# Kernel tuning notes

Measured on AMD Instinct MI355X. Metric: run time of the kernel, lower is better.

Reference implementation:

```python
import jax, jax.numpy as jnp
import numpy as np

N_EX = 50000          # n_exercise
D = 128               # exercise_embed_dim
E = 600000            # number of e2e edges
N = N_EX + 1          # node count: zero pad row + exercises 1..n_exercise


def setup_inputs() -> dict:
    key = jax.random.key(0)
    k1, k2, k3, k4, k5 = jax.random.split(key, 5)
    # learned params
    W_embed = jax.random.normal(k1, (N, D), dtype=jnp.float32) * 0.02   # nn.Embedding(n_exercise+1, D)
    W_gcn = jax.random.normal(k2, (D, D), dtype=jnp.float32) * (1.0 / np.sqrt(D))  # GCNConv lin weight
    b_gcn = jnp.zeros((D,), dtype=jnp.float32)                          # GCNConv bias
    # graph / sequence inputs
    edge_index = jax.random.randint(k3, (2, E), 0, N, dtype=jnp.int64)
    e_inputs = jax.random.randint(k4, (16, 200), 0, N_EX, dtype=jnp.int64)
    a_inputs = jax.random.randint(k5, (16, 200), 0, 2, dtype=jnp.int64)
    return {"W_embed": W_embed, "W_gcn": W_gcn, "b_gcn": b_gcn,
            "edge_index": edge_index, "e_inputs": e_inputs, "a_inputs": a_inputs}


def reference(W_embed, W_gcn, b_gcn, edge_index, e_inputs, a_inputs):
    n_nodes, d = W_embed.shape
    # exercise_embed = embed(arange(1, n_exercise+1)); prepend zero row ->
    # equivalent to the full table with row 0 zeroed.
    x = W_embed.at[0].set(0.0)                        # [N, D]

    # PyG GCNConv: h = x @ W, then D^-1/2 (A + I) D^-1/2 h + b
    h = x @ W_gcn                                     # [N, D]
    src = edge_index[0]
    dst = edge_index[1]
    ones_e = jnp.ones(src.shape[0], dtype=h.dtype)
    # degree including self-loop weight 1
    deg = 1.0 + jax.ops.segment_sum(ones_e, dst, num_segments=n_nodes)  # [N]
    dis = jax.lax.rsqrt(deg)                          # deg^-1/2
    norm = dis[src] * dis[dst]                        # [E]
    msg = h[src] * norm[:, None]                      # gather + scale, [E, D]
    agg = jax.ops.segment_sum(msg, dst, num_segments=n_nodes)           # scatter-add, [N, D]
    agg = agg + h * (1.0 / deg)[:, None]              # self-loop term (norm = 1/deg)
    return agg + b_gcn                                # [N, D]
```

## Files before the change

kernel.cpp:

```cpp
#include <hip/hip_runtime.h>

#define N_NODES 50001
#define DIM 128
#define GEMM_BLOCKS 782
#define CAP 64
#define NB 196
#define FILLB 293
#define EPB 2048
#define BCAP 40
#define GCAPR 640
#define OCAP 8192

typedef __attribute__((ext_vector_type(8))) short short8v;
typedef __attribute__((ext_vector_type(4))) float f32x4;

__device__ __forceinline__ ushort f2bf(float f) {
    unsigned u = __float_as_uint(f);
    unsigned r = (u + 0x7FFF + ((u >> 16) & 1)) >> 16;
    return (ushort)r;
}

__global__ void prep_kernel(int* __restrict__ gcntp, int* __restrict__ ocnt,
                            const float* __restrict__ Wg, ushort* __restrict__ wt) {
    __shared__ float tile[32][36];
    const int t = threadIdx.x;
    if (blockIdx.x == 0) {
        for (int i = t; i < NB * 8 * 16; i += 256) gcntp[i] = 0;
        if (t == 0) *ocnt = 0;
        return;
    }
    const int b2 = blockIdx.x - 1;
    const int bk = b2 >> 2;
    const int bn = b2 & 3;
    {
        int k = bk * 32 + (t >> 3);
        int n = bn * 32 + (t & 7) * 4;
        float4 v = *(const float4*)&Wg[(size_t)k * DIM + n];
        tile[t >> 3][(t & 7) * 4 + 0] = v.x;
        tile[t >> 3][(t & 7) * 4 + 1] = v.y;
        tile[t >> 3][(t & 7) * 4 + 2] = v.z;
        tile[t >> 3][(t & 7) * 4 + 3] = v.w;
    }
    __syncthreads();
    {
        int n = bn * 32 + (t >> 3);
        int k = bk * 32 + (t & 7) * 4;
        ushort4 w4;
        w4.x = f2bf(tile[(t & 7) * 4 + 0][t >> 3]);
        w4.y = f2bf(tile[(t & 7) * 4 + 1][t >> 3]);
        w4.z = f2bf(tile[(t & 7) * 4 + 2][t >> 3]);
        w4.w = f2bf(tile[(t & 7) * 4 + 3][t >> 3]);
        *(ushort4*)&wt[(size_t)n * DIM + k] = w4;
    }
}

__launch_bounds__(256)
__global__ void gemm_fill_kernel(const float* __restrict__ X, const ushort* __restrict__ wt,
                                 ushort* __restrict__ h16,
                                 const int* __restrict__ src, const int* __restrict__ dst,
                                 int E, int* __restrict__ gcntp, int* __restrict__ gbkt,
                                 int* __restrict__ ocnt, int* __restrict__ obkt) {
    __shared__ int lcnt[NB];
    __shared__ int lbkt[NB * BCAP];
    const int bid = blockIdx.x;
    const int t   = threadIdx.x;
    if (bid >= GEMM_BLOCKS) {
        const int fid = bid - GEMM_BLOCKS;
        const int r   = bid & 7;
        for (int i = t; i < NB; i += 256) lcnt[i] = 0;
        __syncthreads();
        const int e0 = fid * EPB;
        const int e1 = min(e0 + EPB, E);
        for (int e = e0 + t; e < e1; e += 256) {
            int d = dst[e];
            int s = src[e];
            int b = d >> 8;
            unsigned en = (unsigned)s | ((unsigned)(d & 255) << 16);
            int pos = atomicAdd(&lcnt[b], 1);
            if (pos < BCAP) lbkt[b * BCAP + pos] = (int)en;
            else {
                int op = atomicAdd(ocnt, 1);
                if (op < OCAP) obkt[op] = (int)(en | ((unsigned)b << 24));
            }
        }
        __syncthreads();
        if (t < NB) {
            int c = min(lcnt[t], BCAP);
            if (c > 0) {
                int gpos = atomicAdd(&gcntp[(t * 8 + r) * 16], c);
                int* gp = &gbkt[(size_t)(t * 8 + r) * GCAPR];
                for (int i = 0; i < c; ++i) {
                    int g = gpos + i;
                    if (g < GCAPR) gp[g] = lbkt[t * BCAP + i];
                    else {
                        int op = atomicAdd(ocnt, 1);
                        if (op < OCAP)
                            obkt[op] = (int)((unsigned)lbkt[t * BCAP + i] | ((unsigned)t << 24));
                    }
                }
            }
        }
        return;
    }
    const int vb   = bid;
    const int l    = t & 63;
    const int wave = t >> 6;
    const int m0   = vb * 64 + wave * 16;
    const int lm   = l & 15;
    const int lg   = l >> 4;

    const int arow  = m0 + lm;
    const bool aok  = (arow > 0) && (arow < N_NODES);
    const int koff0 = lg * 8;

    f32x4 acc[8];
#pragma unroll
    for (int ct = 0; ct < 8; ++ct) acc[ct] = (f32x4){0.f, 0.f, 0.f, 0.f};

#pragma unroll
    for (int kci = 0; kci < 4; ++kci) {
        const int kc = kci * 32;
        float4 v0 = make_float4(0.f, 0.f, 0.f, 0.f), v1 = v0;
        if (aok) {
            const float* xp = &X[(size_t)arow * DIM + kc + koff0];
            v0 = *(const float4*)xp;
            v1 = *(const float4*)(xp + 4);
        }
        short8v a;
        a[0] = (short)f2bf(v0.x); a[1] = (short)f2bf(v0.y);
        a[2] = (short)f2bf(v0.z); a[3] = (short)f2bf(v0.w);
        a[4] = (short)f2bf(v1.x); a[5] = (short)f2bf(v1.y);
        a[6] = (short)f2bf(v1.z); a[7] = (short)f2bf(v1.w);
#pragma unroll
        for (int ct = 0; ct < 8; ++ct) {
            short8v b = *(const short8v*)&wt[(size_t)(ct * 16 + lm) * DIM + kc + koff0];
            acc[ct] = __builtin_amdgcn_mfma_f32_16x16x32_bf16(a, b, acc[ct], 0, 0, 0);
        }
    }

#pragma unroll
    for (int r = 0; r < 4; ++r) {
        int row = m0 + lg * 4 + r;
        if (row < N_NODES) {
            ushort* hp = &h16[(size_t)row * DIM + lm];
#pragma unroll
            for (int ct = 0; ct < 8; ++ct) hp[ct * 16] = f2bf(acc[ct][r]);
        }
    }
}

__launch_bounds__(256)
__global__ void bin_kernel(const int* __restrict__ gcntp, const int* __restrict__ gbkt,
                           const int* __restrict__ ocnt, const int* __restrict__ obkt,
                           ushort* __restrict__ slot, int* __restrict__ deg) {
    __shared__ __align__(16) ushort lslot[256 * CAP];
    __shared__ int ldeg[256];
    const int t = threadIdx.x;
    const int b = blockIdx.x;
    ldeg[t] = 0;
    __syncthreads();

    for (int r = 0; r < 8; ++r) {
        const int cnt = min(gcntp[(b * 8 + r) * 16], GCAPR);
        const int* bp = &gbkt[(size_t)(b * 8 + r) * GCAPR];
        for (int i = t; i < cnt; i += 256) {
            unsigned en = (unsigned)bp[i];
            int dlow = (en >> 16) & 255;
            int pos = atomicAdd(&ldeg[dlow], 1);
            if (pos < CAP) lslot[dlow * CAP + pos] = (ushort)(en & 0xFFFFu);
        }
    }
    const int oc = min(*ocnt, OCAP);
    for (int i = t; i < oc; i += 256) {
        unsigned en = (unsigned)obkt[i];
        if ((int)(en >> 24) == b) {
            int dlow = (en >> 16) & 255;
            int pos = atomicAdd(&ldeg[dlow], 1);
            if (pos < CAP) lslot[dlow * CAP + pos] = (ushort)(en & 0xFFFFu);
        }
    }
    __syncthreads();

    const int node = b * 256 + t;
    if (node < N_NODES) deg[node] = ldeg[t];
    const uint4* ls4 = (const uint4*)lslot;
    uint4* gs4 = (uint4*)&slot[(size_t)b * 256 * CAP];
#pragma unroll
    for (int k = 0; k < 8; ++k) gs4[k * 256 + t] = ls4[k * 256 + t];
}

__launch_bounds__(256)
__global__ void pull_kernel(const int* __restrict__ deg, const ushort* __restrict__ slot,
                            const ushort* __restrict__ h16,
                            const float* __restrict__ b, float* __restrict__ out) {
    const int tid  = threadIdx.x;
    const int lane = tid & 63;
    const int g    = lane >> 4;
    const int c    = lane & 15;
    const int n    = blockIdx.x * 4 + (tid >> 6);
    if (n >= N_NODES) return;

    const int dn_i = deg[n];
    const int end  = min(dn_i, CAP);
    const ushort* sp = &slot[(size_t)n * CAP];

    float ac[8];
#pragma unroll
    for (int j = 0; j < 8; ++j) ac[j] = 0.f;

    int e = g;
    while (e + 4 < end) {
        int s0 = sp[e];
        int s1 = sp[e + 4];
        float d0 = rsqrtf(1.0f + (float)deg[s0]);
        float d1 = rsqrtf(1.0f + (float)deg[s1]);
        uint4 u0 = *(const uint4*)&h16[(size_t)s0 * DIM + c * 8];
        uint4 u1 = *(const uint4*)&h16[(size_t)s1 * DIM + c * 8];
        const unsigned w0[4] = {u0.x, u0.y, u0.z, u0.w};
        const unsigned w1[4] = {u1.x, u1.y, u1.z, u1.w};
#pragma unroll
        for (int p = 0; p < 4; ++p) {
            ac[2*p]   += d0 * __uint_as_float(w0[p] << 16)
                       + d1 * __uint_as_float(w1[p] << 16);
            ac[2*p+1] += d0 * __uint_as_float(w0[p] & 0xFFFF0000u)
                       + d1 * __uint_as_float(w1[p] & 0xFFFF0000u);
        }
        e += 8;
    }
    while (e < end) {
        int s = sp[e];
        float d = rsqrtf(1.0f + (float)deg[s]);
        uint4 u = *(const uint4*)&h16[(size_t)s * DIM + c * 8];
        const unsigned w[4] = {u.x, u.y, u.z, u.w};
#pragma unroll
        for (int p = 0; p < 4; ++p) {
            ac[2*p]   += d * __uint_as_float(w[p] << 16);
            ac[2*p+1] += d * __uint_as_float(w[p] & 0xFFFF0000u);
        }
        e += 4;
    }

#pragma unroll
    for (int j = 0; j < 8; ++j) {
        ac[j] += __shfl_xor(ac[j], 16, 64);
        ac[j] += __shfl_xor(ac[j], 32, 64);
    }

    if (g == 0) {
        const float dn = rsqrtf(1.0f + (float)dn_i);
        uint4 us = *(const uint4*)&h16[(size_t)n * DIM + c * 8];
        const unsigned ws[4] = {us.x, us.y, us.z, us.w};
        float r[8];
#pragma unroll
        for (int p = 0; p < 4; ++p) {
            r[2*p]   = ac[2*p]   + dn * __uint_as_float(ws[p] << 16);
            r[2*p+1] = ac[2*p+1] + dn * __uint_as_float(ws[p] & 0xFFFF0000u);
        }
        float* op = &out[(size_t)n * DIM + c * 8];
        const float* bp = &b[c * 8];
        float4 o0, o1;
        o0.x = dn * r[0] + bp[0]; o0.y = dn * r[1] + bp[1];
        o0.z = dn * r[2] + bp[2]; o0.w = dn * r[3] + bp[3];
        o1.x = dn * r[4] + bp[4]; o1.y = dn * r[5] + bp[5];
        o1.z = dn * r[6] + bp[6]; o1.w = dn * r[7] + bp[7];
        *(float4*)op = o0;
        *(float4*)(op + 4) = o1;
    }
}

extern "C" void kernel_launch(void* const* d_in, const int* in_sizes, int n_in,
                              void* d_out, int out_size, void* d_ws, size_t ws_size,
                              hipStream_t stream) {
    const float* W_embed = (const float*)d_in[0];
    const float* W_gcn   = (const float*)d_in[1];
    const float* b_gcn   = (const float*)d_in[2];
    const int*   edges   = (const int*)d_in[3];
    const int E = in_sizes[3] / 2;
    const int* src = edges;
    const int* dst = edges + E;

    float* out = (float*)d_out;
    char*  ws  = (char*)d_ws;
    int*    gcntp = (int*)ws;
    int*    ocnt  = (int*)(ws + 0x19000);
    int*    obkt  = (int*)(ws + 0x20000);
    ushort* wt    = (ushort*)(ws + 0x28000);
    int*    gbkt  = (int*)(ws + 0x30000);
    ushort* slot  = (ushort*)(ws + 0x500000);
    int*    deg   = (int*)(ws + 0xC00000);
    ushort* h16   = (ushort*)(ws + 0xD00000);

    prep_kernel<<<17, 256, 0, stream>>>(gcntp, ocnt, W_gcn, wt);
    gemm_fill_kernel<<<GEMM_BLOCKS + FILLB, 256, 0, stream>>>(
        W_embed, wt, h16, src, dst, E, gcntp, gbkt, ocnt, obkt);
    bin_kernel<<<NB, 256, 0, stream>>>(gcntp, gbkt, ocnt, obkt, slot, deg);
    pull_kernel<<<(N_NODES + 3) / 4, 256, 0, stream>>>(deg, slot, h16, b_gcn, out);
}
```

Baseline: 72.48 us.

## Fuse bucket binning into pull kernel and compute degrees with global atomics

Merges the bin and pull kernels so each block bins one quarter of a 256-node bucket into LDS slots and aggregates from there directly. This removes the global slot array round trip and one kernel launch. Degrees are now counted with global atomics during the fill phase, because pull needs source-node degrees from other buckets. Each bucket's edge lists are scanned four times (once per quarter block), and the fill phase gains 600k global atomics.

```diff
diff --git a/kernel.cpp b/kernel.cpp
--- a/kernel.cpp
+++ b/kernel.cpp
@@ -10,6 +10,8 @@
 #define BCAP 40
 #define GCAPR 640
 #define OCAP 8192
+#define ZDEG 49
+#define ZG 25
 
 typedef __attribute__((ext_vector_type(8))) short short8v;
 typedef __attribute__((ext_vector_type(4))) float f32x4;
@@ -20,16 +22,23 @@
     return (ushort)r;
 }
 
-__global__ void prep_kernel(int* __restrict__ gcntp, int* __restrict__ ocnt,
+__global__ void prep_kernel(int* __restrict__ deg, int* __restrict__ gcntp,
+                            int* __restrict__ ocnt,
                             const float* __restrict__ Wg, ushort* __restrict__ wt) {
     __shared__ float tile[32][36];
     const int t = threadIdx.x;
-    if (blockIdx.x == 0) {
-        for (int i = t; i < NB * 8 * 16; i += 256) gcntp[i] = 0;
-        if (t == 0) *ocnt = 0;
+    if (blockIdx.x < ZDEG) {
+        int i = blockIdx.x * 256 + t;
+        if (i < 12501) ((uint4*)deg)[i] = make_uint4(0, 0, 0, 0);
         return;
     }
-    const int b2 = blockIdx.x - 1;
+    if (blockIdx.x < ZDEG + ZG) {
+        int i = (blockIdx.x - ZDEG) * 256 + t;
+        if (i < 6272) ((uint4*)gcntp)[i] = make_uint4(0, 0, 0, 0);
+        if (blockIdx.x == ZDEG && t == 0) *ocnt = 0;
+        return;
+    }
+    const int b2 = blockIdx.x - (ZDEG + ZG);
     const int bk = b2 >> 2;
     const int bn = b2 & 3;
     {
@@ -58,7 +67,8 @@
 __global__ void gemm_fill_kernel(const float* __restrict__ X, const ushort* __restrict__ wt,
                                  ushort* __restrict__ h16,
                                  const int* __restrict__ src, const int* __restrict__ dst,
-                                 int E, int* __restrict__ gcntp, int* __restrict__ gbkt,
+                                 int E, int* __restrict__ deg,
+                                 int* __restrict__ gcntp, int* __restrict__ gbkt,
                                  int* __restrict__ ocnt, int* __restrict__ obkt) {
     __shared__ int lcnt[NB];
     __shared__ int lbkt[NB * BCAP];
@@ -76,6 +86,7 @@
             int s = src[e];
             int b = d >> 8;
             unsigned en = (unsigned)s | ((unsigned)(d & 255) << 16);
+            atomicAdd(&deg[d], 1);
             int pos = atomicAdd(&lcnt[b], 1);
             if (pos < BCAP) lbkt[b * BCAP + pos] = (int)en;
             else {
@@ -150,121 +161,120 @@
 }
 
 __launch_bounds__(256)
-__global__ void bin_kernel(const int* __restrict__ gcntp, const int* __restrict__ gbkt,
-                           const int* __restrict__ ocnt, const int* __restrict__ obkt,
-                           ushort* __restrict__ slot, int* __restrict__ deg) {
-    __shared__ __align__(16) ushort lslot[256 * CAP];
-    __shared__ int ldeg[256];
+__global__ void binpull_kernel(const int* __restrict__ gcntp, const int* __restrict__ gbkt,
+                               const int* __restrict__ ocnt, const int* __restrict__ obkt,
+                               const int* __restrict__ deg, const ushort* __restrict__ h16,
+                               const float* __restrict__ bias, float* __restrict__ out) {
+    __shared__ __align__(16) ushort lslot[64 * CAP];
+    __shared__ int lcnt[64];
     const int t = threadIdx.x;
-    const int b = blockIdx.x;
-    ldeg[t] = 0;
+    const int B = blockIdx.x >> 2;
+    const int q = blockIdx.x & 3;
+    if (t < 64) lcnt[t] = 0;
     __syncthreads();
 
     for (int r = 0; r < 8; ++r) {
-        const int cnt = min(gcntp[(b * 8 + r) * 16], GCAPR);
-        const int* bp = &gbkt[(size_t)(b * 8 + r) * GCAPR];
+        const int cnt = min(gcntp[(B * 8 + r) * 16], GCAPR);
+        const int* bp = &gbkt[(size_t)(B * 8 + r) * GCAPR];
         for (int i = t; i < cnt; i += 256) {
             unsigned en = (unsigned)bp[i];
             int dlow = (en >> 16) & 255;
-            int pos = atomicAdd(&ldeg[dlow], 1);
-            if (pos < CAP) lslot[dlow * CAP + pos] = (ushort)(en & 0xFFFFu);
+            if ((dlow >> 6) == q) {
+                int ln = dlow & 63;
+                int pos = atomicAdd(&lcnt[ln], 1);
+                if (pos < CAP) lslot[ln * CAP + pos] = (ushort)(en & 0xFFFFu);
+            }
         }
     }
     const int oc = min(*ocnt, OCAP);
     for (int i = t; i < oc; i += 256) {
         unsigned en = (unsigned)obkt[i];
-        if ((int)(en >> 24) == b) {
+        if ((int)(en >> 24) == B) {
             int dlow = (en >> 16) & 255;
-            int pos = atomicAdd(&ldeg[dlow], 1);
-            if (pos < CAP) lslot[dlow * CAP + pos] = (ushort)(en & 0xFFFFu);
+            if ((dlow >> 6) == q) {
+                int ln = dlow & 63;
+                int pos = atomicAdd(&lcnt[ln], 1);
+                if (pos < CAP) lslot[ln * CAP + pos] = (ushort)(en & 0xFFFFu);
+            }
         }
     }
     __syncthreads();
 
-    const int node = b * 256 + t;
-    if (node < N_NODES) deg[node] = ldeg[t];
-    const uint4* ls4 = (const uint4*)lslot;
-    uint4* gs4 = (uint4*)&slot[(size_t)b * 256 * CAP];
-#pragma unroll
-    for (int k = 0; k < 8; ++k) gs4[k * 256 + t] = ls4[k * 256 + t];
-}
-
-__launch_bounds__(256)
-__global__ void pull_kernel(const int* __restrict__ deg, const ushort* __restrict__ slot,
-                            const ushort* __restrict__ h16,
-                            const float* __restrict__ b, float* __restrict__ out) {
-    const int tid  = threadIdx.x;
-    const int lane = tid & 63;
+    const int lane = t & 63;
+    const int w    = t >> 6;
     const int g    = lane >> 4;
     const int c    = lane & 15;
-    const int n    = blockIdx.x * 4 + (tid >> 6);
-    if (n >= N_NODES) return;
-
-    const int dn_i = deg[n];
-    const int end  = min(dn_i, CAP);
-    const ushort* sp = &slot[(size_t)n * CAP];
-
-    float ac[8];
-#pragma unroll
-    for (int j = 0; j < 8; ++j) ac[j] = 0.f;
-
-    int e = g;
-    while (e + 4 < end) {
-        int s0 = sp[e];
-        int s1 = sp[e + 4];
-        float d0 = rsqrtf(1.0f + (float)deg[s0]);
-        float d1 = rsqrtf(1.0f + (float)deg[s1]);
-        uint4 u0 = *(const uint4*)&h16[(size_t)s0 * DIM + c * 8];
-        uint4 u1 = *(const uint4*)&h16[(size_t)s1 * DIM + c * 8];
-        const unsigned w0[4] = {u0.x, u0.y, u0.z, u0.w};
-        const unsigned w1[4] = {u1.x, u1.y, u1.z, u1.w};
-#pragma unroll
-        for (int p = 0; p < 4; ++p) {
-            ac[2*p]   += d0 * __uint_as_float(w0[p] << 16)
-                       + d1 * __uint_as_float(w1[p] << 16);
-            ac[2*p+1] += d0 * __uint_as_float(w0[p] & 0xFFFF0000u)
-                       + d1 * __uint_as_float(w1[p] & 0xFFFF0000u);
-        }
-        e += 8;
-    }
-    while (e < end) {
-        int s = sp[e];
-        float d = rsqrtf(1.0f + (float)deg[s]);
-        uint4 u = *(const uint4*)&h16[(size_t)s * DIM + c * 8];
-        const unsigned w[4] = {u.x, u.y, u.z, u.w};
-#pragma unroll
-        for (int p = 0; p < 4; ++p) {
-            ac[2*p]   += d * __uint_as_float(w[p] << 16);
-            ac[2*p+1] += d * __uint_as_float(w[p] & 0xFFFF0000u);
-        }
-        e += 4;
-    }
-
-#pragma unroll
-    for (int j = 0; j < 8; ++j) {
-        ac[j] += __shfl_xor(ac[j], 16, 64);
-        ac[j] += __shfl_xor(ac[j], 32, 64);
-    }
-
-    if (g == 0) {
-        const float dn = rsqrtf(1.0f + (float)dn_i);
-        uint4 us = *(const uint4*)&h16[(size_t)n * DIM + c * 8];
-        const unsigned ws[4] = {us.x, us.y, us.z, us.w};
-        float r[8];
-#pragma unroll
-        for (int p = 0; p < 4; ++p) {
-            r[2*p]   = ac[2*p]   + dn * __uint_as_float(ws[p] << 16);
-            r[2*p+1] = ac[2*p+1] + dn * __uint_as_float(ws[p] & 0xFFFF0000u);
-        }
-        float* op = &out[(size_t)n * DIM + c * 8];
-        const float* bp = &b[c * 8];
-        float4 o0, o1;
-        o0.x = dn * r[0] + bp[0]; o0.y = dn * r[1] + bp[1];
-        o0.z = dn * r[2] + bp[2]; o0.w = dn * r[3] + bp[3];
-        o1.x = dn * r[4] + bp[4]; o1.y = dn * r[5] + bp[5];
-        o1.z = dn * r[6] + bp[6]; o1.w = dn * r[7] + bp[7];
-        *(float4*)op = o0;
-        *(float4*)(op + 4) = o1;
+
+    for (int ln = w; ln < 64; ln += 4) {
+        const int n = B * 256 + q * 64 + ln;
+        if (n >= N_NODES) break;
+
+        const int dn_i = lcnt[ln];
+        const int end  = min(dn_i, CAP);
+        const ushort* sp = &lslot[ln * CAP];
+
+        float ac[8];
+#pragma unroll
+        for (int j = 0; j < 8; ++j) ac[j] = 0.f;
+
+        int e = g;
+        while (e + 4 < end) {
+            int s0 = sp[e];
+            int s1 = sp[e + 4];
+            float d0 = rsqrtf(1.0f + (float)deg[s0]);
+            float d1 = rsqrtf(1.0f + (float)deg[s1]);
+            uint4 u0 = *(const uint4*)&h16[(size_t)s0 * DIM + c * 8];
+            uint4 u1 = *(const uint4*)&h16[(size_t)s1 * DIM + c * 8];
+            const unsigned w0[4] = {u0.x, u0.y, u0.z, u0.w};
+            const unsigned w1[4] = {u1.x, u1.y, u1.z, u1.w};
+#pragma unroll
+            for (int p = 0; p < 4; ++p) {
+                ac[2*p]   += d0 * __uint_as_float(w0[p] << 16)
+                           + d1 * __uint_as_float(w1[p] << 16);
+                ac[2*p+1] += d0 * __uint_as_float(w0[p] & 0xFFFF0000u)
+                           + d1 * __uint_as_float(w1[p] & 0xFFFF0000u);
+            }
+            e += 8;
+        }
+        while (e < end) {
+            int s = sp[e];
+            float d = rsqrtf(1.0f + (float)deg[s]);
+            uint4 u = *(const uint4*)&h16[(size_t)s * DIM + c * 8];
+            const unsigned wv[4] = {u.x, u.y, u.z, u.w};
+#pragma unroll
+            for (int p = 0; p < 4; ++p) {
+                ac[2*p]   += d * __uint_as_float(wv[p] << 16);
+                ac[2*p+1] += d * __uint_as_float(wv[p] & 0xFFFF0000u);
+            }
+            e += 4;
+        }
+
+#pragma unroll
+        for (int j = 0; j < 8; ++j) {
+            ac[j] += __shfl_xor(ac[j], 16, 64);
+            ac[j] += __shfl_xor(ac[j], 32, 64);
+        }
+
+        if (g == 0) {
+            const float dn = rsqrtf(1.0f + (float)dn_i);
+            uint4 us = *(const uint4*)&h16[(size_t)n * DIM + c * 8];
+            const unsigned wsr[4] = {us.x, us.y, us.z, us.w};
+            float r[8];
+#pragma unroll
+            for (int p = 0; p < 4; ++p) {
+                r[2*p]   = ac[2*p]   + dn * __uint_as_float(wsr[p] << 16);
+                r[2*p+1] = ac[2*p+1] + dn * __uint_as_float(wsr[p] & 0xFFFF0000u);
+            }
+            float* op = &out[(size_t)n * DIM + c * 8];
+            const float* bp = &bias[c * 8];
+            float4 o0, o1;
+            o0.x = dn * r[0] + bp[0]; o0.y = dn * r[1] + bp[1];
+            o0.z = dn * r[2] + bp[2]; o0.w = dn * r[3] + bp[3];
+            o1.x = dn * r[4] + bp[4]; o1.y = dn * r[5] + bp[5];
+            o1.z = dn * r[6] + bp[6]; o1.w = dn * r[7] + bp[7];
+            *(float4*)op = o0;
+            *(float4*)(op + 4) = o1;
+        }
     }
 }
 
@@ -286,13 +296,11 @@
     int*    obkt  = (int*)(ws + 0x20000);
     ushort* wt    = (ushort*)(ws + 0x28000);
     int*    gbkt  = (int*)(ws + 0x30000);
-    ushort* slot  = (ushort*)(ws + 0x500000);
-    int*    deg   = (int*)(ws + 0xC00000);
-    ushort* h16   = (ushort*)(ws + 0xD00000);
-
-    prep_kernel<<<17, 256, 0, stream>>>(gcntp, ocnt, W_gcn, wt);
+    int*    deg   = (int*)(ws + 0x500000);
+    ushort* h16   = (ushort*)(ws + 0x600000);
+
+    prep_kernel<<<ZDEG + ZG + 16, 256, 0, stream>>>(deg, gcntp, ocnt, W_gcn, wt);
     gemm_fill_kernel<<<GEMM_BLOCKS + FILLB, 256, 0, stream>>>(
-        W_embed, wt, h16, src, dst, E, gcntp, gbkt, ocnt, obkt);
-    bin_kernel<<<NB, 256, 0, stream>>>(gcntp, gbkt, ocnt, obkt, slot, deg);
-    pull_kernel<<<(N_NODES + 3) / 4, 256, 0, stream>>>(deg, slot, h16, b_gcn, out);
-}
+        W_embed, wt, h16, src, dst, E, deg, gcntp, gbkt, ocnt, obkt);
+    binpull_kernel<<<NB * 4, 256, 0, stream>>>(gcntp, gbkt, ocnt, obkt, deg, h16, b_gcn, out);
+}
```

New measurement: 91.52 us. +26.3%, slower.
